# Performance work log

Hardware: AMD Instinct MI355X
Metric: run time of the kernel (lower is better)

## Reference

```python
import jax, jax.numpy as jnp
import numpy as np

B = 256
NUM_ROUTES = 32 * 6 * 6  # 1152
NUM_CAPS = 10
OUT_CH = 16
IN_CH = 8


def squash(x, axis=-1):
    sq = jnp.sum(x * x, axis=axis, keepdims=True)
    return sq * x / ((1.0 + sq) * jnp.sqrt(sq))


def conv2d(x, w, b, stride):
    y = jax.lax.conv_general_dilated(
        x, w, window_strides=(stride, stride), padding='VALID',
        dimension_numbers=('NCHW', 'OIHW', 'NCHW'))
    return y + b[None, :, None, None]


def setup_inputs() -> dict:
    key = jax.random.key(0)
    ks = jax.random.split(key, 12)
    data = jax.random.normal(ks[0], (B, 1, 28, 28), dtype=jnp.float32)
    conv1_w = jax.random.normal(ks[1], (256, 1, 9, 9), dtype=jnp.float32) * 0.1
    conv1_b = jax.random.normal(ks[2], (256,), dtype=jnp.float32) * 0.01
    # 8 primary-capsule convs, each 256->32, k9 s2 (stacked)
    pc_w = jax.random.normal(ks[3], (8, 32, 256, 9, 9), dtype=jnp.float32) * 0.02
    pc_b = jax.random.normal(ks[4], (8, 32), dtype=jnp.float32) * 0.01
    # DigitCaps routing weights (torch.randn init)
    W_dc = jax.random.normal(ks[5], (NUM_ROUTES, NUM_CAPS, OUT_CH, IN_CH), dtype=jnp.float32)
    dec_w1 = jax.random.normal(ks[6], (160, 512), dtype=jnp.float32) * 0.05
    dec_b1 = jnp.zeros((512,), dtype=jnp.float32)
    dec_w2 = jax.random.normal(ks[7], (512, 1024), dtype=jnp.float32) * 0.05
    dec_b2 = jnp.zeros((1024,), dtype=jnp.float32)
    dec_w3 = jax.random.normal(ks[8], (1024, 784), dtype=jnp.float32) * 0.05
    dec_b3 = jnp.zeros((784,), dtype=jnp.float32)
    return dict(data=data, conv1_w=conv1_w, conv1_b=conv1_b, pc_w=pc_w, pc_b=pc_b,
                W_dc=W_dc, dec_w1=dec_w1, dec_b1=dec_b1, dec_w2=dec_w2,
                dec_b2=dec_b2, dec_w3=dec_w3, dec_b3=dec_b3)


def capsnet_forward(data, conv1_w, conv1_b, pc_w, pc_b, W_dc,
                    dec_w1, dec_b1, dec_w2, dec_b2, dec_w3, dec_b3):
    bsz = data.shape[0]
    # ConvLayer: [B,1,28,28] -> [B,256,20,20]
    x = jax.nn.relu(conv2d(data, conv1_w, conv1_b, 1))
    # PrimaryCaps: 8 independent convs fused into one 256-out conv then split
    # [B,256,6,6] viewed as [B,8,32,6,6] matches torch.stack(u, dim=1)
    u = conv2d(x, pc_w.reshape(256, 256, 9, 9), pc_b.reshape(256), 2)
    u = u.reshape(bsz, NUM_ROUTES, IN_CH)  # [B,1152,8]
    u = squash(u)
    # DigitCaps: u_hat[b,r,c,o] = sum_i W[r,c,o,i] * u[b,r,i]
    u_hat = jnp.einsum('rcoi,bri->brco', W_dc, u)  # [B,1152,10,16]
    b_ij = jnp.zeros((NUM_ROUTES, NUM_CAPS), dtype=u_hat.dtype)
    num_iterations = 3
    v = None
    for it in range(num_iterations):
        c_ij = jax.nn.softmax(b_ij, axis=0)            # softmax over routes
        s_j = jnp.einsum('rc,brco->bco', c_ij, u_hat)  # [B,10,16]
        v = squash(s_j, axis=-1)
        if it < num_iterations - 1:
            a_ij = jnp.einsum('brco,bco->rc', u_hat, v) / bsz  # mean over batch
            b_ij = b_ij + a_ij
    output = v[..., None]  # [B,10,16,1]
    # Decoder
    classes = jnp.sqrt(jnp.sum(output ** 2, axis=2))   # [B,10,1]
    classes = jax.nn.softmax(classes, axis=0)          # softmax over batch (as in source)
    idx = jnp.argmax(classes, axis=1)[:, 0]            # [B]
    masked = jnp.eye(NUM_CAPS, dtype=output.dtype)[idx]  # [B,10]
    t = (output * masked[:, :, None, None]).reshape(bsz, -1)  # [B,160]
    h = jax.nn.relu(t @ dec_w1 + dec_b1)
    h = jax.nn.relu(h @ dec_w2 + dec_b2)
    recon = jax.nn.sigmoid(h @ dec_w3 + dec_b3).reshape(bsz, 1, 28, 28)
    return output, recon, masked


def reference(data, conv1_w, conv1_b, pc_w, pc_b, W_dc,
              dec_w1, dec_b1, dec_w2, dec_b2, dec_w3, dec_b3):
    return capsnet_forward(data, conv1_w, conv1_b, pc_w, pc_b, W_dc,
                           dec_w1, dec_b1, dec_w2, dec_b2, dec_w3, dec_b3)
```

## Files before the change

kernel.cpp:

```cpp
#include <hip/hip_runtime.h>
#include <math.h>


typedef __attribute__((ext_vector_type(8))) short short8;
typedef __attribute__((ext_vector_type(4))) float f32x4;

__device__ __forceinline__ unsigned short f2bf(float x) {
  unsigned int u = __float_as_uint(x);
  unsigned int r = (u + 0x7fffu + ((u >> 16) & 1u)) >> 16;
  return (unsigned short)r;
}
__device__ __forceinline__ float bf2f(unsigned short h) {
  return __uint_as_float(((unsigned int)h) << 16);
}
__device__ __forceinline__ void gload16(const void* g, void* l) {
  __builtin_amdgcn_global_load_lds(
      (const __attribute__((address_space(1))) unsigned int*)g,
      (__attribute__((address_space(3))) unsigned int*)l, 16, 0, 0);
}
__device__ __forceinline__ float dot8(const float* w, float4 a, float4 b) {
  return w[0]*a.x + w[1]*a.y + w[2]*a.z + w[3]*a.w +
         w[4]*b.x + w[5]*b.y + w[6]*b.z + w[7]*b.w;
}

__global__ __launch_bounds__(320) void conv1_kernel(
    const float* __restrict__ data, const float* __restrict__ w1,
    const float* __restrict__ b1, unsigned short* __restrict__ xh,
    unsigned short* __restrict__ xl)
{
  const int bid = blockIdx.x;
  const int b   = bid >> 2;
  const int cog = bid & 3;
  __shared__ float img[784];
  __shared__ float wsm[81][64];
  const int t = threadIdx.x;
  for (int i = t; i < 784; i += 320) img[i] = data[b * 784 + i];
  for (int i = t; i < 64 * 81; i += 320) {
    int col = i / 81, k = i % 81;
    wsm[k][col] = w1[(cog * 64 + col) * 81 + k];
  }
  __syncthreads();
  const int cg = t & 15;
  const int oy = t >> 4;
  const int co0 = cog * 64 + cg * 4;
  float acc[4][20];
  #pragma unroll
  for (int i = 0; i < 4; i++) {
    float bv = b1[co0 + i];
    #pragma unroll
    for (int j = 0; j < 20; j++) acc[i][j] = bv;
  }
  for (int ky = 0; ky < 9; ky++) {
    float xr[28];
    const float4* rp = reinterpret_cast<const float4*>(&img[(oy + ky) * 28]);
    #pragma unroll
    for (int q = 0; q < 7; q++) {
      float4 v4 = rp[q];
      xr[q*4+0] = v4.x; xr[q*4+1] = v4.y; xr[q*4+2] = v4.z; xr[q*4+3] = v4.w;
    }
    #pragma unroll
    for (int kx = 0; kx < 9; kx++) {
      float4 wv = *reinterpret_cast<const float4*>(&wsm[ky * 9 + kx][cg * 4]);
      #pragma unroll
      for (int ox = 0; ox < 20; ox++) {
        float xv = xr[ox + kx];
        acc[0][ox] = fmaf(xv, wv.x, acc[0][ox]);
        acc[1][ox] = fmaf(xv, wv.y, acc[1][ox]);
        acc[2][ox] = fmaf(xv, wv.z, acc[2][ox]);
        acc[3][ox] = fmaf(xv, wv.w, acc[3][ox]);
      }
    }
  }
  #pragma unroll
  for (int ox = 0; ox < 20; ox++) {
    ushort4 hv, lv;
    float v0 = fmaxf(acc[0][ox], 0.f), v1 = fmaxf(acc[1][ox], 0.f);
    float v2 = fmaxf(acc[2][ox], 0.f), v3 = fmaxf(acc[3][ox], 0.f);
    hv.x = f2bf(v0); lv.x = f2bf(v0 - bf2f(hv.x));
    hv.y = f2bf(v1); lv.y = f2bf(v1 - bf2f(hv.y));
    hv.z = f2bf(v2); lv.z = f2bf(v2 - bf2f(hv.z));
    hv.w = f2bf(v3); lv.w = f2bf(v3 - bf2f(hv.w));
    const int pix = (b * 20 + oy) * 20 + ox;
    *(ushort4*)(xh + pix * 256 + co0) = hv;
    *(ushort4*)(xl + pix * 256 + co0) = lv;
  }
}

__global__ void wprep(const float* __restrict__ pw, unsigned short* __restrict__ wh,
                      unsigned short* __restrict__ wl)
{
  const int co = blockIdx.x;
  const int t  = threadIdx.x;
  __shared__ float slab[20736];
  for (int i = t; i < 20736; i += 256) slab[i] = pw[co * 20736 + i];
  __syncthreads();
  const int cc = t >> 5, ci5 = t & 31;
  for (int k = 0; k < 81; k++) {
    float x = slab[t * 81 + k];
    unsigned short h = f2bf(x);
    int dst = ((k * 8 + cc) * 256 + co) * 32 + ci5;
    wh[dst] = h;
    wl[dst] = f2bf(x - bf2f(h));
  }
}

__global__ __launch_bounds__(256) void conv2_mfma(
    const unsigned short* __restrict__ xh, const unsigned short* __restrict__ xl,
    const unsigned short* __restrict__ wh, const unsigned short* __restrict__ wl,
    float* __restrict__ part)
{
  __shared__ char lds[24576];
  const int t   = threadIdx.x;
  const int blk = blockIdx.x;
  const int mt  = blk % 144;
  const int kg  = blk / 144;
  const int m0  = mt * 64;
  const int lane = t & 63;
  const int w    = t >> 6;
  const int l15  = lane & 15, l4 = lane >> 4;

  const int ib2 = ((t >> 2) ^ (t >> 4)) & 1;
  const int ib1 = ((t >> 1) ^ (t >> 3)) & 1;
  const int ib0 = (t ^ (t >> 2) ^ (t >> 4)) & 1;
  const int g   = (t & ~7) | (ib2 << 2) | (ib1 << 1) | ib0;
  const int ar  = g >> 2, ach = g & 3;
  const int apix = m0 + ar;
  const int ab  = apix / 36;
  const int asp = apix - ab * 36;
  const int aoy = asp / 6;
  const int aox = asp - aoy * 6;
  const int abase = ((ab * 20 + 2 * aoy) * 20 + 2 * aox) * 256 + ach * 8;

  const int bofs = (w * 64 + l15) * 32 + l4 * 8;

  f32x4 acc[4][4];
  #pragma unroll
  for (int i = 0; i < 4; i++)
    #pragma unroll
    for (int j = 0; j < 4; j++) acc[i][j] = (f32x4){0.f, 0.f, 0.f, 0.f};

  const int ky0 = kg * 3;

  auto stageA = [&](int buf, int axy) {
    char* base = lds + buf * 8192;
    gload16(xh + abase + axy, base + t * 16);
    gload16(xl + abase + axy, base + 4096 + t * 16);
  };

  stageA(0, (ky0 * 20) * 256);
  int kyc = ky0, kxc = 0, ccc = 0;
  #pragma unroll 1
  for (int s = 0; s < 216; ++s) {
    const int slab = ((kyc * 9 + kxc) * 8 + ccc) * 8192;
    const unsigned short* bhp = wh + slab + bofs;
    const unsigned short* blp = wl + slab + bofs;
    short8 b_h[4], b_l[4];
    #pragma unroll
    for (int nf = 0; nf < 4; nf++) {
      b_h[nf] = *(const short8*)(bhp + nf * 512);
      b_l[nf] = *(const short8*)(blp + nf * 512);
    }
    ccc++;
    if (ccc == 8) { ccc = 0; kxc++; if (kxc == 9) { kxc = 0; kyc++; } }
    if (s < 215) {
      stageA((s + 1) % 3, (kyc * 20 + kxc) * 256 + ccc * 32);
      asm volatile("s_waitcnt vmcnt(10)" ::: "memory");
    } else {
      asm volatile("s_waitcnt vmcnt(8)" ::: "memory");
    }
    asm volatile("s_barrier" ::: "memory");

    char* base = lds + (s % 3) * 8192;
    short8 a_h[4], a_l[4];
    #pragma unroll
    for (int mf = 0; mf < 4; mf++) {
      const int row = mf * 16 + l15;
      const int off = ((((row << 2) | l4) ^ (l15 & 7)) << 4);
      a_h[mf] = *(const short8*)(base + off);
      a_l[mf] = *(const short8*)(base + 4096 + off);
    }
    __builtin_amdgcn_s_setprio(1);
    #pragma unroll
    for (int nf = 0; nf < 4; nf++)
      #pragma unroll
      for (int mf = 0; mf < 4; mf++) {
        f32x4 a = acc[mf][nf];
        a = __builtin_amdgcn_mfma_f32_16x16x32_bf16(a_h[mf], b_h[nf], a, 0, 0, 0);
        a = __builtin_amdgcn_mfma_f32_16x16x32_bf16(a_l[mf], b_h[nf], a, 0, 0, 0);
        a = __builtin_amdgcn_mfma_f32_16x16x32_bf16(a_h[mf], b_l[nf], a, 0, 0, 0);
        acc[mf][nf] = a;
      }
    __builtin_amdgcn_s_setprio(0);
    asm volatile("s_waitcnt lgkmcnt(0)" ::: "memory");
  }

  float* pout = part + kg * 2359296;
  #pragma unroll
  for (int mf = 0; mf < 4; mf++)
    #pragma unroll
    for (int nf = 0; nf < 4; nf++) {
      const int co = w * 64 + nf * 16 + l15;
      #pragma unroll
      for (int reg = 0; reg < 4; reg++) {
        const int pix = m0 + mf * 16 + l4 * 4 + reg;
        const int b  = pix / 36;
        const int sp = pix - b * 36;
        pout[b * 9216 + co * 36 + sp] = acc[mf][nf][reg];
      }
    }
}

__global__ void combine_squash(const float* __restrict__ part,
                               const float* __restrict__ pb,
                               float* __restrict__ uT)
{
  const int id = blockIdx.x * 256 + threadIdx.x;
  const int b = id / 1152;
  const int r = id % 1152;
  const float* p0 = part + b * 9216 + r * 8;
  float v[8];
  #pragma unroll
  for (int i = 0; i < 8; i++) v[i] = p0[i] + p0[2359296 + i] + p0[4718592 + i];
  #pragma unroll
  for (int i = 0; i < 8; i++) v[i] += pb[(r * 8 + i) / 36];
  float sq = 0.f;
  #pragma unroll
  for (int i = 0; i < 8; i++) sq += v[i] * v[i];
  float scale = sq / ((1.f + sq) * sqrtf(sq));
  #pragma unroll
  for (int i = 0; i < 8; i++) uT[(r * 256 + b) * 8 + i] = v[i] * scale;
}

__global__ __launch_bounds__(256) void s_pass(
    const float* __restrict__ uT, const float* __restrict__ Wdc,
    const float* __restrict__ bij, float* __restrict__ spart, int uniform)
{
  const int c  = blockIdx.x % 10;
  const int q  = blockIdx.x / 10;
  const int r0 = q * 18;
  const int t  = threadIdx.x;
  __shared__ float wsm[18 * 128];
  __shared__ float cw[18];
  __shared__ float red[8];

  #pragma unroll
  for (int k = 0; k < 9; k++) {
    int idx = t + k * 256;
    int r = idx >> 7, i = idx & 127;
    wsm[idx] = Wdc[((r0 + r) * 10 + c) * 128 + i];
  }
  if (uniform) {
    if (t < 18) cw[t] = 1.f / 1152.f;
  } else {
    float bv[5]; float m = -1e30f;
    #pragma unroll
    for (int rr = 0; rr < 5; rr++) {
      int r = t + rr * 256;
      bv[rr] = (r < 1152) ? bij[c * 1152 + r] : -1e30f;
      m = fmaxf(m, bv[rr]);
    }
    #pragma unroll
    for (int off = 32; off; off >>= 1) m = fmaxf(m, __shfl_down(m, off, 64));
    if ((t & 63) == 0) red[t >> 6] = m;
    __syncthreads();
    m = fmaxf(fmaxf(red[0], red[1]), fmaxf(red[2], red[3]));
    float ssum = 0.f;
    #pragma unroll
    for (int rr = 0; rr < 5; rr++)
      ssum += (t + rr * 256 < 1152) ? expf(bv[rr] - m) : 0.f;
    #pragma unroll
    for (int off = 32; off; off >>= 1) ssum += __shfl_down(ssum, off, 64);
    if ((t & 63) == 0) red[4 + (t >> 6)] = ssum;
    __syncthreads();
    float inv = 1.f / (red[4] + red[5] + red[6] + red[7]);
    if (t < 18) cw[t] = expf(bij[c * 1152 + r0 + t] - m) * inv;
  }
  __syncthreads();

  const float4* up = (const float4*)(uT + (r0 * 256 + t) * 8);
  float acc[16];
  #pragma unroll
  for (int o = 0; o < 16; o++) acc[o] = 0.f;
  #pragma unroll 1
  for (int r = 0; r < 18; r++) {
    float4 x0 = up[r * 512], x1 = up[r * 512 + 1];
    float cwr = cw[r];
    const float* wr = &wsm[r * 128];
    #pragma unroll
    for (int o = 0; o < 16; o++) {
      const float4 wa = *(const float4*)(wr + o * 8);
      const float4 wb = *(const float4*)(wr + o * 8 + 4);
      acc[o] += cwr * (wa.x*x0.x + wa.y*x0.y + wa.z*x0.z + wa.w*x0.w
                     + wb.x*x1.x + wb.y*x1.y + wb.z*x1.z + wb.w*x1.w);
    }
  }
  float* op = spart + q * 40960 + (t * 10 + c) * 16;
  #pragma unroll
  for (int o = 0; o < 16; o++) op[o] = acc[o];
}

template <int FINAL>
__global__ void reduce_squash(const float* __restrict__ spart, float* __restrict__ outb)
{
  const int id = blockIdx.x * 256 + threadIdx.x;
  float a = 0.f;
  #pragma unroll 8
  for (int q = 0; q < 64; q++) a += spart[q * 40960 + id];
  if (FINAL) { outb[id] = a; return; }
  float sq = a * a;
  #pragma unroll
  for (int off = 8; off; off >>= 1) sq += __shfl_xor(sq, off, 16);
  float scale = sq / ((1.f + sq) * sqrtf(sq));
  const int bc = id >> 4, o = id & 15;
  const int b = bc / 10, c = bc - b * 10;
  outb[(c * 256 + b) * 16 + o] = a * scale;
}

__global__ __launch_bounds__(256) void a_pass(
    const float* __restrict__ uT, const float* __restrict__ W,
    const float* __restrict__ vT, float* __restrict__ bij, int assign)
{
  const int r = blockIdx.x;
  const int t = threadIdx.x;
  __shared__ float wsl[1280];
  __shared__ float lred[4][10];
  for (int i = t; i < 1280; i += 256) wsl[i] = W[r * 1280 + i];
  __syncthreads();
  const float4* up = (const float4*)(uT + (r * 256 + t) * 8);
  float4 ua = up[0], ub = up[1];
  const int lane = t & 63, wid = t >> 6;
  #pragma unroll 1
  for (int c = 0; c < 10; c++) {
    const float* wc = &wsl[c * 128];
    const float4* vp = (const float4*)(vT + (c * 256 + t) * 16);
    float p = 0.f;
    #pragma unroll
    for (int q = 0; q < 4; q++) {
      float4 vq = vp[q];
      p += dot8(wc + (q * 4 + 0) * 8, ua, ub) * vq.x;
      p += dot8(wc + (q * 4 + 1) * 8, ua, ub) * vq.y;
      p += dot8(wc + (q * 4 + 2) * 8, ua, ub) * vq.z;
      p += dot8(wc + (q * 4 + 3) * 8, ua, ub) * vq.w;
    }
    for (int off = 32; off; off >>= 1) p += __shfl_down(p, off, 64);
    if (lane == 0) lred[wid][c] = p;
  }
  __syncthreads();
  if (t < 10) {
    float a = (lred[0][t] + lred[1][t] + lred[2][t] + lred[3][t]) * (1.f / 256.f);
    float o = assign ? 0.f : bij[t * 1152 + r];
    bij[t * 1152 + r] = o + a;
  }
}

__global__ __launch_bounds__(256) void finalize(
    const float* __restrict__ sbuf, float* __restrict__ outp,
    float* __restrict__ maskedo, float* __restrict__ tbuf)
{
  const int b = threadIdx.x;
  __shared__ float nsm[256][10];
  __shared__ float red[8];
  #pragma unroll 1
  for (int c = 0; c < 10; c++) {
    const float4* sp = (const float4*)(sbuf + (b * 10 + c) * 16);
    float4 q0 = sp[0], q1 = sp[1], q2 = sp[2], q3 = sp[3];
    float sq = q0.x*q0.x+q0.y*q0.y+q0.z*q0.z+q0.w*q0.w
             + q1.x*q1.x+q1.y*q1.y+q1.z*q1.z+q1.w*q1.w
             + q2.x*q2.x+q2.y*q2.y+q2.z*q2.z+q2.w*q2.w
             + q3.x*q3.x+q3.y*q3.y+q3.z*q3.z+q3.w*q3.w;
    float scale = sq / ((1.f + sq) * sqrtf(sq));
    float4* op = (float4*)(outp + (b * 10 + c) * 16);
    op[0] = make_float4(q0.x*scale, q0.y*scale, q0.z*scale, q0.w*scale);
    op[1] = make_float4(q1.x*scale, q1.y*scale, q1.z*scale, q1.w*scale);
    op[2] = make_float4(q2.x*scale, q2.y*scale, q2.z*scale, q2.w*scale);
    op[3] = make_float4(q3.x*scale, q3.y*scale, q3.z*scale, q3.w*scale);
    nsm[b][c] = sq / (1.f + sq);
  }
  __syncthreads();
  float sc[10];
  #pragma unroll
  for (int c = 0; c < 10; c++) {
    float x = nsm[b][c];
    float m = x;
    #pragma unroll
    for (int off = 32; off; off >>= 1) m = fmaxf(m, __shfl_down(m, off, 64));
    if ((b & 63) == 0) red[b >> 6] = m;
    __syncthreads();
    m = fmaxf(fmaxf(red[0], red[1]), fmaxf(red[2], red[3]));
    float e = expf(x - m), ss = e;
    #pragma unroll
    for (int off = 32; off; off >>= 1) ss += __shfl_down(ss, off, 64);
    if ((b & 63) == 0) red[4 + (b >> 6)] = ss;
    __syncthreads();
    sc[c] = e / (red[4] + red[5] + red[6] + red[7]);
    __syncthreads();
  }
  int idx = 0; float best = sc[0];
  #pragma unroll
  for (int c = 1; c < 10; c++) if (sc[c] > best) { best = sc[c]; idx = c; }
  #pragma unroll
  for (int c = 0; c < 10; c++) {
    float msk = (c == idx) ? 1.f : 0.f;
    maskedo[b * 10 + c] = msk;
    const float4* op = (const float4*)(outp + (b * 10 + c) * 16);
    float4* tp = (float4*)(tbuf + b * 160 + c * 16);
    #pragma unroll
    for (int qq = 0; qq < 4; qq++) {
      float4 vv = op[qq];
      tp[qq] = make_float4(vv.x * msk, vv.y * msk, vv.z * msk, vv.w * msk);
    }
  }
}

template <int ACT>
__global__ __launch_bounds__(256) void gemm_act(
    const float* __restrict__ A, const float* __restrict__ B,
    const float* __restrict__ bias, float* __restrict__ C, int M, int N, int K)
{
  __shared__ float As[64][17];
  __shared__ float Bs[16][64];
  const int t = threadIdx.x;
  const int tx = t & 15, ty = t >> 4;
  const int m0 = blockIdx.y * 64, n0 = blockIdx.x * 64;
  float acc[4][4] = {};
  for (int kb = 0; kb < K; kb += 16) {
    {
      int row = t >> 2, c4 = (t & 3) * 4;
      float4 av = *(const float4*)(A + (m0 + row) * K + kb + c4);
      As[row][c4+0]=av.x; As[row][c4+1]=av.y; As[row][c4+2]=av.z; As[row][c4+3]=av.w;
    }
    {
      int row = t >> 4, c4 = (t & 15) * 4;
      float4 bv = make_float4(0.f, 0.f, 0.f, 0.f);
      if (n0 + c4 < N) bv = *(const float4*)(B + (kb + row) * N + n0 + c4);
      Bs[row][c4+0]=bv.x; Bs[row][c4+1]=bv.y; Bs[row][c4+2]=bv.z; Bs[row][c4+3]=bv.w;
    }
    __syncthreads();
    #pragma unroll
    for (int kk = 0; kk < 16; kk++) {
      float a_[4], b_[4];
      #pragma unroll
      for (int i = 0; i < 4; i++) a_[i] = As[ty * 4 + i][kk];
      #pragma unroll
      for (int j = 0; j < 4; j++) b_[j] = Bs[kk][tx * 4 + j];
      #pragma unroll
      for (int i = 0; i < 4; i++)
        for (int j = 0; j < 4; j++)
          acc[i][j] = fmaf(a_[i], b_[j], acc[i][j]);
    }
    __syncthreads();
  }
  #pragma unroll
  for (int i = 0; i < 4; i++) {
    int row = m0 + ty * 4 + i;
    #pragma unroll
    for (int j = 0; j < 4; j++) {
      int col = n0 + tx * 4 + j;
      if (col < N) {
        float val = acc[i][j] + bias[col];
        if (ACT == 0) val = val > 0.f ? val : 0.f;
        else          val = 1.f / (1.f + expf(-val));
        C[row * N + col] = val;
      }
    }
  }
}

extern "C" void kernel_launch(void* const* d_in, const int* in_sizes, int n_in,
                              void* d_out, int out_size, void* d_ws, size_t ws_size,
                              hipStream_t stream)
{
  const float* data = (const float*)d_in[0];
  const float* w1   = (const float*)d_in[1];
  const float* b1   = (const float*)d_in[2];
  const float* pw   = (const float*)d_in[3];
  const float* pb   = (const float*)d_in[4];
  const float* Wdc  = (const float*)d_in[5];
  const float* dw1  = (const float*)d_in[6];
  const float* db1  = (const float*)d_in[7];
  const float* dw2  = (const float*)d_in[8];
  const float* db2  = (const float*)d_in[9];
  const float* dw3  = (const float*)d_in[10];
  const float* db3  = (const float*)d_in[11];

  float* out     = (float*)d_out;
  float* outp    = out;
  float* recon   = out + 40960;
  float* maskedo = out + 241664;

  char* wsb = (char*)d_ws;
  unsigned short* x1h = (unsigned short*)(wsb);
  unsigned short* x1l = (unsigned short*)(wsb + 52428800);
  unsigned short* wbh = (unsigned short*)(wsb + 104857600);
  unsigned short* wbl = (unsigned short*)(wsb + 115474432);
  float*  part = (float*)(wsb + 126091264);
  float* uT   = (float*)(wsb);
  float* vT   = (float*)(wsb + 9437184);
  float* bij  = (float*)(wsb + 9601024);
  float* sbuf = (float*)(wsb + 9647104);
  float* spart= (float*)(wsb + 9810944);
  float* tbuf = (float*)(wsb + 20296704);
  float* h1   = (float*)(wsb + 20460544);
  float* h2   = (float*)(wsb + 20984832);

  conv1_kernel<<<1024, 320, 0, stream>>>(data, w1, b1, x1h, x1l);
  wprep<<<256, 256, 0, stream>>>(pw, wbh, wbl);
  conv2_mfma<<<432, 256, 0, stream>>>(x1h, x1l, wbh, wbl, part);
  combine_squash<<<1152, 256, 0, stream>>>(part, pb, uT);

  s_pass<<<640, 256, 0, stream>>>(uT, Wdc, bij, spart, 1);
  reduce_squash<0><<<160, 256, 0, stream>>>(spart, vT);
  a_pass<<<1152, 256, 0, stream>>>(uT, Wdc, vT, bij, 1);
  s_pass<<<640, 256, 0, stream>>>(uT, Wdc, bij, spart, 0);
  reduce_squash<0><<<160, 256, 0, stream>>>(spart, vT);
  a_pass<<<1152, 256, 0, stream>>>(uT, Wdc, vT, bij, 0);
  s_pass<<<640, 256, 0, stream>>>(uT, Wdc, bij, spart, 0);
  reduce_squash<1><<<160, 256, 0, stream>>>(spart, sbuf);
  finalize<<<1, 256, 0, stream>>>(sbuf, outp, maskedo, tbuf);

  gemm_act<0><<<dim3(8, 4),  256, 0, stream>>>(tbuf, dw1, db1, h1,    256, 512,  160);
  gemm_act<0><<<dim3(16, 4), 256, 0, stream>>>(h1,   dw2, db2, h2,    256, 1024, 512);
  gemm_act<1><<<dim3(13, 4), 256, 0, stream>>>(h2,   dw3, db3, recon, 256, 784,  1024);
}
```

Before: 692.9 us.

## Recast routing s-pass as split-bf16 MFMA GEMM and double conv2 K-step

The routing s-step becomes a GEMM. The softmax coefficients are folded into the DigitCaps weights, which are split into bf16 hi/lo parts. A new MFMA kernel then multiplies these by hi/lo splits of u over K=9216, replacing the scalar FMA s_pass. Separately, the conv2 MFMA kernel stages two 32-channel slices per iteration with a 48KB LDS triple buffer, halving barriers and loop iterations. The changes add extra kernels (route_softmax, wcsplit) and higher LDS use, which may reduce occupancy.

```diff
diff --git a/kernel.cpp b/kernel.cpp
--- a/kernel.cpp
+++ b/kernel.cpp
@@ -109,7 +109,7 @@
     const unsigned short* __restrict__ wh, const unsigned short* __restrict__ wl,
     float* __restrict__ part)
 {
-  __shared__ char lds[24576];
+  __shared__ char lds[49152];
   const int t   = threadIdx.x;
   const int blk = blockIdx.x;
   const int mt  = blk % 144;
@@ -119,17 +119,16 @@
   const int w    = t >> 6;
   const int l15  = lane & 15, l4 = lane >> 4;
 
-  const int ib2 = ((t >> 2) ^ (t >> 4)) & 1;
-  const int ib1 = ((t >> 1) ^ (t >> 3)) & 1;
-  const int ib0 = (t ^ (t >> 2) ^ (t >> 4)) & 1;
-  const int g   = (t & ~7) | (ib2 << 2) | (ib1 << 1) | ib0;
-  const int ar  = g >> 2, ach = g & 3;
-  const int apix = m0 + ar;
-  const int ab  = apix / 36;
-  const int asp = apix - ab * 36;
-  const int aoy = asp / 6;
-  const int aox = asp - aoy * 6;
-  const int abase = ((ab * 20 + 2 * aoy) * 20 + 2 * aox) * 256 + ach * 8;
+  const int g0  = t ^ ((t >> 3) & 7);
+  const int ar0 = g0 >> 3;
+  const int ach = g0 & 7;
+  auto pixbase = [&](int pix) {
+    int ab = pix / 36; int sp = pix - ab * 36;
+    int oy = sp / 6;   int ox = sp - oy * 6;
+    return ((ab * 20 + 2 * oy) * 20 + 2 * ox) * 256;
+  };
+  const int abase0 = pixbase(m0 + ar0) + ach * 8;
+  const int abase1 = pixbase(m0 + ar0 + 32) + ach * 8;
 
   const int bofs = (w * 64 + l15) * 32 + l4 * 8;
 
@@ -141,57 +140,63 @@
 
   const int ky0 = kg * 3;
 
-  auto stageA = [&](int buf, int axy) {
-    char* base = lds + buf * 8192;
-    gload16(xh + abase + axy, base + t * 16);
-    gload16(xl + abase + axy, base + 4096 + t * 16);
+  auto stageA = [&](int buf, int xy, int ci0) {
+    char* base = lds + buf * 16384;
+    gload16(xh + abase0 + xy + ci0, base + t * 16);
+    gload16(xh + abase1 + xy + ci0, base + 4096  + t * 16);
+    gload16(xl + abase0 + xy + ci0, base + 8192  + t * 16);
+    gload16(xl + abase1 + xy + ci0, base + 12288 + t * 16);
   };
 
-  stageA(0, (ky0 * 20) * 256);
-  int kyc = ky0, kxc = 0, ccc = 0;
+  stageA(0, ky0 * 20 * 256, 0);
+  int kyc = ky0, kxc = 0, cc2 = 0;
   #pragma unroll 1
-  for (int s = 0; s < 216; ++s) {
-    const int slab = ((kyc * 9 + kxc) * 8 + ccc) * 8192;
-    const unsigned short* bhp = wh + slab + bofs;
-    const unsigned short* blp = wl + slab + bofs;
-    short8 b_h[4], b_l[4];
-    #pragma unroll
-    for (int nf = 0; nf < 4; nf++) {
-      b_h[nf] = *(const short8*)(bhp + nf * 512);
-      b_l[nf] = *(const short8*)(blp + nf * 512);
-    }
-    ccc++;
-    if (ccc == 8) { ccc = 0; kxc++; if (kxc == 9) { kxc = 0; kyc++; } }
-    if (s < 215) {
-      stageA((s + 1) % 3, (kyc * 20 + kxc) * 256 + ccc * 32);
-      asm volatile("s_waitcnt vmcnt(10)" ::: "memory");
+  for (int s = 0; s < 108; ++s) {
+    const int kkc = (kyc * 9 + kxc) * 8 + cc2 * 2;
+    short8 b_h[4][2], b_l[4][2];
+    #pragma unroll
+    for (int ks = 0; ks < 2; ks++) {
+      const unsigned short* bhp = wh + (kkc + ks) * 8192 + bofs;
+      const unsigned short* blp = wl + (kkc + ks) * 8192 + bofs;
+      #pragma unroll
+      for (int nf = 0; nf < 4; nf++) {
+        b_h[nf][ks] = *(const short8*)(bhp + nf * 512);
+        b_l[nf][ks] = *(const short8*)(blp + nf * 512);
+      }
+    }
+    cc2++; if (cc2 == 4) { cc2 = 0; kxc++; if (kxc == 9) { kxc = 0; kyc++; } }
+    if (s < 107) {
+      stageA((s + 1) % 3, (kyc * 20 + kxc) * 256, cc2 * 64);
+      asm volatile("s_waitcnt vmcnt(20)" ::: "memory");
     } else {
-      asm volatile("s_waitcnt vmcnt(8)" ::: "memory");
+      asm volatile("s_waitcnt vmcnt(16)" ::: "memory");
     }
     asm volatile("s_barrier" ::: "memory");
 
-    char* base = lds + (s % 3) * 8192;
-    short8 a_h[4], a_l[4];
-    #pragma unroll
-    for (int mf = 0; mf < 4; mf++) {
-      const int row = mf * 16 + l15;
-      const int off = ((((row << 2) | l4) ^ (l15 & 7)) << 4);
-      a_h[mf] = *(const short8*)(base + off);
-      a_l[mf] = *(const short8*)(base + 4096 + off);
-    }
-    __builtin_amdgcn_s_setprio(1);
-    #pragma unroll
-    for (int nf = 0; nf < 4; nf++)
+    char* base = lds + (s % 3) * 16384;
+    #pragma unroll
+    for (int ks = 0; ks < 2; ks++) {
+      short8 a_h[4], a_l[4];
       #pragma unroll
       for (int mf = 0; mf < 4; mf++) {
-        f32x4 a = acc[mf][nf];
-        a = __builtin_amdgcn_mfma_f32_16x16x32_bf16(a_h[mf], b_h[nf], a, 0, 0, 0);
-        a = __builtin_amdgcn_mfma_f32_16x16x32_bf16(a_l[mf], b_h[nf], a, 0, 0, 0);
-        a = __builtin_amdgcn_mfma_f32_16x16x32_bf16(a_h[mf], b_l[nf], a, 0, 0, 0);
-        acc[mf][nf] = a;
+        const int row = mf * 16 + l15;
+        const int off = ((row * 8 + ks * 4 + l4) ^ (l15 & 7)) << 4;
+        a_h[mf] = *(const short8*)(base + off);
+        a_l[mf] = *(const short8*)(base + 8192 + off);
       }
-    __builtin_amdgcn_s_setprio(0);
-    asm volatile("s_waitcnt lgkmcnt(0)" ::: "memory");
+      __builtin_amdgcn_s_setprio(1);
+      #pragma unroll
+      for (int nf = 0; nf < 4; nf++)
+        #pragma unroll
+        for (int mf = 0; mf < 4; mf++) {
+          f32x4 a = acc[mf][nf];
+          a = __builtin_amdgcn_mfma_f32_16x16x32_bf16(a_h[mf], b_h[nf][ks], a, 0, 0, 0);
+          a = __builtin_amdgcn_mfma_f32_16x16x32_bf16(a_l[mf], b_h[nf][ks], a, 0, 0, 0);
+          a = __builtin_amdgcn_mfma_f32_16x16x32_bf16(a_h[mf], b_l[nf][ks], a, 0, 0, 0);
+          acc[mf][nf] = a;
+        }
+      __builtin_amdgcn_s_setprio(0);
+    }
   }
 
   float* pout = part + kg * 2359296;
@@ -212,7 +217,9 @@
 
 __global__ void combine_squash(const float* __restrict__ part,
                                const float* __restrict__ pb,
-                               float* __restrict__ uT)
+                               float* __restrict__ uT,
+                               unsigned short* __restrict__ uBh,
+                               unsigned short* __restrict__ uBl)
 {
   const int id = blockIdx.x * 256 + threadIdx.x;
   const int b = id / 1152;
@@ -227,76 +234,121 @@
   #pragma unroll
   for (int i = 0; i < 8; i++) sq += v[i] * v[i];
   float scale = sq / ((1.f + sq) * sqrtf(sq));
-  #pragma unroll
-  for (int i = 0; i < 8; i++) uT[(r * 256 + b) * 8 + i] = v[i] * scale;
-}
-
-__global__ __launch_bounds__(256) void s_pass(
-    const float* __restrict__ uT, const float* __restrict__ Wdc,
-    const float* __restrict__ bij, float* __restrict__ spart, int uniform)
-{
+  ushort4 hq[2], lq[2];
+  #pragma unroll
+  for (int i = 0; i < 8; i++) {
+    float o = v[i] * scale;
+    uT[(r * 256 + b) * 8 + i] = o;
+    unsigned short h = f2bf(o);
+    ((unsigned short*)hq)[i] = h;
+    ((unsigned short*)lq)[i] = f2bf(o - bf2f(h));
+  }
+  *(ushort4*)(uBh + b * 9216 + r * 8)     = hq[0];
+  *(ushort4*)(uBh + b * 9216 + r * 8 + 4) = hq[1];
+  *(ushort4*)(uBl + b * 9216 + r * 8)     = lq[0];
+  *(ushort4*)(uBl + b * 9216 + r * 8 + 4) = lq[1];
+}
+
+__global__ void route_softmax(const float* __restrict__ bij, float* __restrict__ cij)
+{
+  const int c = blockIdx.x;
+  const int t = threadIdx.x;
+  __shared__ float red[8];
+  float m = -1e30f;
+  for (int r = t; r < 1152; r += 256) m = fmaxf(m, bij[c * 1152 + r]);
+  for (int off = 32; off; off >>= 1) m = fmaxf(m, __shfl_down(m, off, 64));
+  if ((t & 63) == 0) red[t >> 6] = m;
+  __syncthreads();
+  m = fmaxf(fmaxf(red[0], red[1]), fmaxf(red[2], red[3]));
+  float s = 0.f;
+  for (int r = t; r < 1152; r += 256) {
+    float e = expf(bij[c * 1152 + r] - m);
+    cij[c * 1152 + r] = e;
+    s += e;
+  }
+  for (int off = 32; off; off >>= 1) s += __shfl_down(s, off, 64);
+  if ((t & 63) == 0) red[4 + (t >> 6)] = s;
+  __syncthreads();
+  float inv = 1.f / (red[4] + red[5] + red[6] + red[7]);
+  for (int r = t; r < 1152; r += 256) cij[c * 1152 + r] *= inv;
+}
+
+__global__ void wcsplit(const float* __restrict__ Wdc, const float* __restrict__ cij,
+                        unsigned short* __restrict__ Wch, unsigned short* __restrict__ Wcl,
+                        int uniform)
+{
+  const int rb = blockIdx.x / 10;
   const int c  = blockIdx.x % 10;
-  const int q  = blockIdx.x / 10;
-  const int r0 = q * 18;
+  const int r0 = rb * 64;
   const int t  = threadIdx.x;
-  __shared__ float wsm[18 * 128];
-  __shared__ float cw[18];
-  __shared__ float red[8];
-
-  #pragma unroll
-  for (int k = 0; k < 9; k++) {
-    int idx = t + k * 256;
-    int r = idx >> 7, i = idx & 127;
-    wsm[idx] = Wdc[((r0 + r) * 10 + c) * 128 + i];
-  }
-  if (uniform) {
-    if (t < 18) cw[t] = 1.f / 1152.f;
-  } else {
-    float bv[5]; float m = -1e30f;
-    #pragma unroll
-    for (int rr = 0; rr < 5; rr++) {
-      int r = t + rr * 256;
-      bv[rr] = (r < 1152) ? bij[c * 1152 + r] : -1e30f;
-      m = fmaxf(m, bv[rr]);
-    }
-    #pragma unroll
-    for (int off = 32; off; off >>= 1) m = fmaxf(m, __shfl_down(m, off, 64));
-    if ((t & 63) == 0) red[t >> 6] = m;
-    __syncthreads();
-    m = fmaxf(fmaxf(red[0], red[1]), fmaxf(red[2], red[3]));
-    float ssum = 0.f;
-    #pragma unroll
-    for (int rr = 0; rr < 5; rr++)
-      ssum += (t + rr * 256 < 1152) ? expf(bv[rr] - m) : 0.f;
-    #pragma unroll
-    for (int off = 32; off; off >>= 1) ssum += __shfl_down(ssum, off, 64);
-    if ((t & 63) == 0) red[4 + (t >> 6)] = ssum;
-    __syncthreads();
-    float inv = 1.f / (red[4] + red[5] + red[6] + red[7]);
-    if (t < 18) cw[t] = expf(bij[c * 1152 + r0 + t] - m) * inv;
-  }
-  __syncthreads();
-
-  const float4* up = (const float4*)(uT + (r0 * 256 + t) * 8);
-  float acc[16];
-  #pragma unroll
-  for (int o = 0; o < 16; o++) acc[o] = 0.f;
-  #pragma unroll 1
-  for (int r = 0; r < 18; r++) {
-    float4 x0 = up[r * 512], x1 = up[r * 512 + 1];
-    float cwr = cw[r];
-    const float* wr = &wsm[r * 128];
-    #pragma unroll
-    for (int o = 0; o < 16; o++) {
-      const float4 wa = *(const float4*)(wr + o * 8);
-      const float4 wb = *(const float4*)(wr + o * 8 + 4);
-      acc[o] += cwr * (wa.x*x0.x + wa.y*x0.y + wa.z*x0.z + wa.w*x0.w
-                     + wb.x*x1.x + wb.y*x1.y + wb.z*x1.z + wb.w*x1.w);
-    }
-  }
-  float* op = spart + q * 40960 + (t * 10 + c) * 16;
-  #pragma unroll
-  for (int o = 0; o < 16; o++) op[o] = acc[o];
+  __shared__ float slab[64][128];
+  for (int idx = t; idx < 8192; idx += 256) {
+    int r = idx >> 7, oi = idx & 127;
+    float cw = uniform ? (1.f / 1152.f) : cij[c * 1152 + r0 + r];
+    slab[r][oi] = Wdc[((r0 + r) * 10 + c) * 128 + oi] * cw;
+  }
+  __syncthreads();
+  const int o = t >> 4, rr = t & 15;
+  #pragma unroll
+  for (int j = 0; j < 4; j++) {
+    int r = rr + j * 16;
+    short8 hv, lv;
+    #pragma unroll
+    for (int i = 0; i < 8; i++) {
+      float x = slab[r][o * 8 + i];
+      unsigned short h = f2bf(x);
+      hv[i] = (short)h;
+      lv[i] = (short)f2bf(x - bf2f(h));
+    }
+    const int dst = (c * 16 + o) * 9216 + (r0 + r) * 8;
+    *(short8*)(Wch + dst) = hv;
+    *(short8*)(Wcl + dst) = lv;
+  }
+}
+
+__global__ __launch_bounds__(256) void s_gemm(
+    const unsigned short* __restrict__ uBh, const unsigned short* __restrict__ uBl,
+    const unsigned short* __restrict__ Wch, const unsigned short* __restrict__ Wcl,
+    float* __restrict__ spart)
+{
+  const int bid = blockIdx.x;
+  const int mt = bid & 3, kq = bid >> 2;
+  const int t = threadIdx.x, lane = t & 63, w = t >> 6;
+  const int l15 = lane & 15, l4 = lane >> 4;
+  const int b0 = mt * 64 + w * 16;
+  const int k0 = kq * 128;
+  f32x4 acc[10];
+  #pragma unroll
+  for (int nf = 0; nf < 10; nf++) acc[nf] = (f32x4){0.f, 0.f, 0.f, 0.f};
+  const unsigned short* aph = uBh + (b0 + l15) * 9216 + k0 + l4 * 8;
+  const unsigned short* apl = uBl + (b0 + l15) * 9216 + k0 + l4 * 8;
+  const unsigned short* bph = Wch + l15 * 9216 + k0 + l4 * 8;
+  const unsigned short* bpl = Wcl + l15 * 9216 + k0 + l4 * 8;
+  #pragma unroll
+  for (int kk = 0; kk < 4; kk++) {
+    short8 ah = *(const short8*)(aph + kk * 32);
+    short8 al = *(const short8*)(apl + kk * 32);
+    #pragma unroll
+    for (int nf = 0; nf < 10; nf++) {
+      short8 bh = *(const short8*)(bph + nf * 16 * 9216 + kk * 32);
+      short8 bl = *(const short8*)(bpl + nf * 16 * 9216 + kk * 32);
+      f32x4 a = acc[nf];
+      a = __builtin_amdgcn_mfma_f32_16x16x32_bf16(ah, bh, a, 0, 0, 0);
+      a = __builtin_amdgcn_mfma_f32_16x16x32_bf16(al, bh, a, 0, 0, 0);
+      a = __builtin_amdgcn_mfma_f32_16x16x32_bf16(ah, bl, a, 0, 0, 0);
+      acc[nf] = a;
+    }
+  }
+  float* op = spart + kq * 40960;
+  #pragma unroll
+  for (int nf = 0; nf < 10; nf++) {
+    const int n = nf * 16 + l15;
+    #pragma unroll
+    for (int reg = 0; reg < 4; reg++) {
+      const int b = b0 + l4 * 4 + reg;
+      op[b * 160 + n] = acc[nf][reg];
+    }
+  }
 }
 
 template <int FINAL>
@@ -305,15 +357,14 @@
   const int id = blockIdx.x * 256 + threadIdx.x;
   float a = 0.f;
   #pragma unroll 8
-  for (int q = 0; q < 64; q++) a += spart[q * 40960 + id];
+  for (int q = 0; q < 72; q++) a += spart[q * 40960 + id];
   if (FINAL) { outb[id] = a; return; }
   float sq = a * a;
   #pragma unroll
   for (int off = 8; off; off >>= 1) sq += __shfl_xor(sq, off, 16);
   float scale = sq / ((1.f + sq) * sqrtf(sq));
-  const int bc = id >> 4, o = id & 15;
-  const int b = bc / 10, c = bc - b * 10;
-  outb[(c * 256 + b) * 16 + o] = a * scale;
+  const int b = id / 160, n = id - b * 160;
+  outb[((n >> 4) * 256 + b) * 16 + (n & 15)] = a * scale;
 }
 
 __global__ __launch_bounds__(256) void a_pass(
@@ -494,27 +545,37 @@
   unsigned short* wbh = (unsigned short*)(wsb + 104857600);
   unsigned short* wbl = (unsigned short*)(wsb + 115474432);
   float*  part = (float*)(wsb + 126091264);
-  float* uT   = (float*)(wsb);
-  float* vT   = (float*)(wsb + 9437184);
-  float* bij  = (float*)(wsb + 9601024);
-  float* sbuf = (float*)(wsb + 9647104);
-  float* spart= (float*)(wsb + 9810944);
-  float* tbuf = (float*)(wsb + 20296704);
-  float* h1   = (float*)(wsb + 20460544);
-  float* h2   = (float*)(wsb + 20984832);
+  float* uT            = (float*)(wsb);
+  unsigned short* uBh  = (unsigned short*)(wsb + 9437184);
+  unsigned short* uBl  = (unsigned short*)(wsb + 14155776);
+  float* vT   = (float*)(wsb + 18874368);
+  float* bij  = (float*)(wsb + 19038208);
+  float* cij  = (float*)(wsb + 19084288);
+  float* sbuf = (float*)(wsb + 19130368);
+  unsigned short* Wch  = (unsigned short*)(wsb + 19294208);
+  unsigned short* Wcl  = (unsigned short*)(wsb + 22243328);
+  float* spart= (float*)(wsb + 25192448);
+  float* tbuf = (float*)(wsb + 36988928);
+  float* h1   = (float*)(wsb + 37152768);
+  float* h2   = (float*)(wsb + 37677056);
 
   conv1_kernel<<<1024, 320, 0, stream>>>(data, w1, b1, x1h, x1l);
   wprep<<<256, 256, 0, stream>>>(pw, wbh, wbl);
   conv2_mfma<<<432, 256, 0, stream>>>(x1h, x1l, wbh, wbl, part);
-  combine_squash<<<1152, 256, 0, stream>>>(part, pb, uT);
-
-  s_pass<<<640, 256, 0, stream>>>(uT, Wdc, bij, spart, 1);
+  combine_squash<<<1152, 256, 0, stream>>>(part, pb, uT, uBh, uBl);
+
+  wcsplit<<<180, 256, 0, stream>>>(Wdc, cij, Wch, Wcl, 1);
+  s_gemm<<<288, 256, 0, stream>>>(uBh, uBl, Wch, Wcl, spart);
   reduce_squash<0><<<160, 256, 0, stream>>>(spart, vT);
   a_pass<<<1152, 256, 0, stream>>>(uT, Wdc, vT, bij, 1);
-  s_pass<<<640, 256, 0, stream>>>(uT, Wdc, bij, spart, 0);
+  route_softmax<<<10, 256, 0, stream>>>(bij, cij);
+  wcsplit<<<180, 256, 0, stream>>>(Wdc, cij, Wch, Wcl, 0);
+  s_gemm<<<288, 256, 0, stream>>>(uBh, uBl, Wch, Wcl, spart);
   reduce_squash<0><<<160, 256, 0, stream>>>(spart, vT);
   a_pass<<<1152, 256, 0, stream>>>(uT, Wdc, vT, bij, 0);
-  s_pass<<<640, 256, 0, stream>>>(uT, Wdc, bij, spart, 0);
+  route_softmax<<<10, 256, 0, stream>>>(bij, cij);
+  wcsplit<<<180, 256, 0, stream>>>(Wdc, cij, Wch, Wcl, 0);
+  s_gemm<<<288, 256, 0, stream>>>(uBh, uBl, Wch, Wcl, spart);
   reduce_squash<1><<<160, 256, 0, stream>>>(spart, sbuf);
   finalize<<<1, 256, 0, stream>>>(sbuf, outp, maskedo, tbuf);
 
```

Measured after the change: 725.4 us. +4.7%, slower.

## Enlarge conv2 MFMA block tile to 128 pixels with 8 waves and K-step 64

Applied to the files above, without the earlier changes.

The primary-capsule conv kernel now uses 512-thread blocks covering 128 output pixels by 256 channels. Each pipeline stage stages a 64-deep K slice, so there are half as many barriers, and the A tile is loaded once and shared by twice as many waves. LDS moves to a 96KB dynamic triple buffer with a new XOR swizzle, and the per-iteration lgkmcnt wait is removed. The grid shrinks from 432 to 216 blocks, which may leave some compute units idle. The large dynamic LDS request also depends on the launch accepting more than 64KB without an explicit attribute.

```diff
diff --git a/kernel.cpp b/kernel.cpp
--- a/kernel.cpp
+++ b/kernel.cpp
@@ -104,34 +104,33 @@
   }
 }
 
-__global__ __launch_bounds__(256) void conv2_mfma(
+__global__ __launch_bounds__(512) void conv2_mfma(
     const unsigned short* __restrict__ xh, const unsigned short* __restrict__ xl,
     const unsigned short* __restrict__ wh, const unsigned short* __restrict__ wl,
     float* __restrict__ part)
 {
-  __shared__ char lds[24576];
+  extern __shared__ char lds[];
   const int t   = threadIdx.x;
   const int blk = blockIdx.x;
-  const int mt  = blk % 144;
-  const int kg  = blk / 144;
-  const int m0  = mt * 64;
+  const int mt  = blk % 72;
+  const int kg  = blk / 72;
+  const int m0  = mt * 128;
   const int lane = t & 63;
   const int w    = t >> 6;
   const int l15  = lane & 15, l4 = lane >> 4;
-
-  const int ib2 = ((t >> 2) ^ (t >> 4)) & 1;
-  const int ib1 = ((t >> 1) ^ (t >> 3)) & 1;
-  const int ib0 = (t ^ (t >> 2) ^ (t >> 4)) & 1;
-  const int g   = (t & ~7) | (ib2 << 2) | (ib1 << 1) | ib0;
-  const int ar  = g >> 2, ach = g & 3;
-  const int apix = m0 + ar;
-  const int ab  = apix / 36;
-  const int asp = apix - ab * 36;
-  const int aoy = asp / 6;
-  const int aox = asp - aoy * 6;
-  const int abase = ((ab * 20 + 2 * aoy) * 20 + 2 * aox) * 256 + ach * 8;
-
-  const int bofs = (w * 64 + l15) * 32 + l4 * 8;
+  const int mh = w >> 2, nw = w & 3;
+
+  const int g0   = t ^ ((t >> 3) & 7);
+  const int row0 = g0 >> 3, ch = g0 & 7;
+  auto pixbase = [&](int pix) {
+    int ab = pix / 36; int sp = pix - ab * 36;
+    int oy = sp / 6;   int ox = sp - oy * 6;
+    return ((ab * 20 + 2 * oy) * 20 + 2 * ox) * 256;
+  };
+  const int abase0 = pixbase(m0 + row0) + ch * 8;
+  const int abase1 = pixbase(m0 + row0 + 64) + ch * 8;
+
+  const int bofs = (nw * 64 + l15) * 32 + l4 * 8;
 
   f32x4 acc[4][4];
   #pragma unroll
@@ -141,68 +140,74 @@
 
   const int ky0 = kg * 3;
 
-  auto stageA = [&](int buf, int axy) {
-    char* base = lds + buf * 8192;
-    gload16(xh + abase + axy, base + t * 16);
-    gload16(xl + abase + axy, base + 4096 + t * 16);
+  auto stageA = [&](int buf, int xy, int ci0) {
+    char* base = lds + buf * 32768;
+    gload16(xh + abase0 + xy + ci0, base + t * 16);
+    gload16(xh + abase1 + xy + ci0, base + 8192  + t * 16);
+    gload16(xl + abase0 + xy + ci0, base + 16384 + t * 16);
+    gload16(xl + abase1 + xy + ci0, base + 24576 + t * 16);
   };
 
-  stageA(0, (ky0 * 20) * 256);
-  int kyc = ky0, kxc = 0, ccc = 0;
+  stageA(0, ky0 * 20 * 256, 0);
+  int kyc = ky0, kxc = 0, cc2 = 0;
   #pragma unroll 1
-  for (int s = 0; s < 216; ++s) {
-    const int slab = ((kyc * 9 + kxc) * 8 + ccc) * 8192;
-    const unsigned short* bhp = wh + slab + bofs;
-    const unsigned short* blp = wl + slab + bofs;
-    short8 b_h[4], b_l[4];
+  for (int s = 0; s < 108; ++s) {
+    const int kkc = (kyc * 9 + kxc) * 8 + cc2 * 2;
+    short8 b_h[4][2], b_l[4][2];
+    #pragma unroll
+    for (int ks = 0; ks < 2; ks++) {
+      const unsigned short* bhp = wh + (kkc + ks) * 8192 + bofs;
+      const unsigned short* blp = wl + (kkc + ks) * 8192 + bofs;
+      #pragma unroll
+      for (int nf = 0; nf < 4; nf++) {
+        b_h[nf][ks] = *(const short8*)(bhp + nf * 512);
+        b_l[nf][ks] = *(const short8*)(blp + nf * 512);
+      }
+    }
+    cc2++; if (cc2 == 4) { cc2 = 0; kxc++; if (kxc == 9) { kxc = 0; kyc++; } }
+    if (s < 107) {
+      stageA((s + 1) % 3, (kyc * 20 + kxc) * 256, cc2 * 64);
+      asm volatile("s_waitcnt vmcnt(20)" ::: "memory");
+    } else {
+      asm volatile("s_waitcnt vmcnt(16)" ::: "memory");
+    }
+    asm volatile("s_barrier" ::: "memory");
+
+    char* base = lds + (s % 3) * 32768;
+    #pragma unroll
+    for (int ks = 0; ks < 2; ks++) {
+      short8 a_h[4], a_l[4];
+      #pragma unroll
+      for (int mf = 0; mf < 4; mf++) {
+        const int row = mh * 64 + mf * 16 + l15;
+        const int off = ((row * 8 + ks * 4 + l4) ^ (row & 7)) << 4;
+        a_h[mf] = *(const short8*)(base + off);
+        a_l[mf] = *(const short8*)(base + 16384 + off);
+      }
+      __builtin_amdgcn_s_setprio(1);
+      #pragma unroll
+      for (int nf = 0; nf < 4; nf++)
+        #pragma unroll
+        for (int mf = 0; mf < 4; mf++) {
+          f32x4 a = acc[mf][nf];
+          a = __builtin_amdgcn_mfma_f32_16x16x32_bf16(a_h[mf], b_h[nf][ks], a, 0, 0, 0);
+          a = __builtin_amdgcn_mfma_f32_16x16x32_bf16(a_l[mf], b_h[nf][ks], a, 0, 0, 0);
+          a = __builtin_amdgcn_mfma_f32_16x16x32_bf16(a_h[mf], b_l[nf][ks], a, 0, 0, 0);
+          acc[mf][nf] = a;
+        }
+      __builtin_amdgcn_s_setprio(0);
+    }
+  }
+
+  float* pout = part + kg * 2359296;
+  #pragma unroll
+  for (int mf = 0; mf < 4; mf++)
     #pragma unroll
     for (int nf = 0; nf < 4; nf++) {
-      b_h[nf] = *(const short8*)(bhp + nf * 512);
-      b_l[nf] = *(const short8*)(blp + nf * 512);
-    }
-    ccc++;
-    if (ccc == 8) { ccc = 0; kxc++; if (kxc == 9) { kxc = 0; kyc++; } }
-    if (s < 215) {
-      stageA((s + 1) % 3, (kyc * 20 + kxc) * 256 + ccc * 32);
-      asm volatile("s_waitcnt vmcnt(10)" ::: "memory");
-    } else {
-      asm volatile("s_waitcnt vmcnt(8)" ::: "memory");
-    }
-    asm volatile("s_barrier" ::: "memory");
-
-    char* base = lds + (s % 3) * 8192;
-    short8 a_h[4], a_l[4];
-    #pragma unroll
-    for (int mf = 0; mf < 4; mf++) {
-      const int row = mf * 16 + l15;
-      const int off = ((((row << 2) | l4) ^ (l15 & 7)) << 4);
-      a_h[mf] = *(const short8*)(base + off);
-      a_l[mf] = *(const short8*)(base + 4096 + off);
-    }
-    __builtin_amdgcn_s_setprio(1);
-    #pragma unroll
-    for (int nf = 0; nf < 4; nf++)
-      #pragma unroll
-      for (int mf = 0; mf < 4; mf++) {
-        f32x4 a = acc[mf][nf];
-        a = __builtin_amdgcn_mfma_f32_16x16x32_bf16(a_h[mf], b_h[nf], a, 0, 0, 0);
-        a = __builtin_amdgcn_mfma_f32_16x16x32_bf16(a_l[mf], b_h[nf], a, 0, 0, 0);
-        a = __builtin_amdgcn_mfma_f32_16x16x32_bf16(a_h[mf], b_l[nf], a, 0, 0, 0);
-        acc[mf][nf] = a;
-      }
-    __builtin_amdgcn_s_setprio(0);
-    asm volatile("s_waitcnt lgkmcnt(0)" ::: "memory");
-  }
-
-  float* pout = part + kg * 2359296;
-  #pragma unroll
-  for (int mf = 0; mf < 4; mf++)
-    #pragma unroll
-    for (int nf = 0; nf < 4; nf++) {
-      const int co = w * 64 + nf * 16 + l15;
+      const int co = nw * 64 + nf * 16 + l15;
       #pragma unroll
       for (int reg = 0; reg < 4; reg++) {
-        const int pix = m0 + mf * 16 + l4 * 4 + reg;
+        const int pix = m0 + mh * 64 + mf * 16 + l4 * 4 + reg;
         const int b  = pix / 36;
         const int sp = pix - b * 36;
         pout[b * 9216 + co * 36 + sp] = acc[mf][nf][reg];
@@ -505,7 +510,7 @@
 
   conv1_kernel<<<1024, 320, 0, stream>>>(data, w1, b1, x1h, x1l);
   wprep<<<256, 256, 0, stream>>>(pw, wbh, wbl);
-  conv2_mfma<<<432, 256, 0, stream>>>(x1h, x1l, wbh, wbl, part);
+  conv2_mfma<<<216, 512, 98304, stream>>>(x1h, x1l, wbh, wbl, part);
   combine_squash<<<1152, 256, 0, stream>>>(part, pb, uT);
 
   s_pass<<<640, 256, 0, stream>>>(uT, Wdc, bij, spart, 1);
```

Result: slower. 724.2 us (+4.5%).
